# Performance work log

Measured on AMD Instinct MI355X. Metric: run time of the kernel, lower is better.

The kernel has to match this reference:

```python
import jax, jax.numpy as jnp
import numpy as np

N_NODES = 65536
IN_DIM = 256
HIDDEN = 256
NUM_GRAPHS = 128   # B = batch.max()+1; fixed by construction in setup_inputs
MAX_LEN = 1024     # >= max per-graph length (avg 512, binomial tail << 1024)


def _uniform(key, shape, scale):
    return jax.random.uniform(key, shape, jnp.float32, -scale, scale)


def setup_inputs() -> dict:
    key = jax.random.key(0)
    ks = jax.random.split(key, 12)
    x = jax.random.normal(ks[0], (N_NODES, IN_DIM), jnp.float32)
    batch = jnp.sort(jax.random.randint(ks[1], (N_NODES,), 0, NUM_GRAPHS)).astype(jnp.int64)
    s = 1.0 / np.sqrt(HIDDEN)  # torch nn.GRU init: U(-1/sqrt(H), 1/sqrt(H))
    # gate order follows torch: (r, z, n) stacked along first axis -> 3H rows
    params = {
        'W_ih0': _uniform(ks[2], (3 * HIDDEN, IN_DIM), s),
        'W_hh0': _uniform(ks[3], (3 * HIDDEN, HIDDEN), s),
        'b_ih0': _uniform(ks[4], (3 * HIDDEN,), s),
        'b_hh0': _uniform(ks[5], (3 * HIDDEN,), s),
        'W_ih1': _uniform(ks[6], (3 * HIDDEN, HIDDEN), s),
        'W_hh1': _uniform(ks[7], (3 * HIDDEN, HIDDEN), s),
        'b_ih1': _uniform(ks[8], (3 * HIDDEN,), s),
        'b_hh1': _uniform(ks[9], (3 * HIDDEN,), s),
    }
    return {'x': x, 'batch': batch, **params}


def _gru_layer(xs, W_ih, W_hh, b_ih, b_hh):
    # xs: [B, L, D] -> [B, L, H]; torch GRU cell math, gate order (r, z, n)
    B = xs.shape[0]
    H = W_hh.shape[1]
    gx = jnp.einsum('bld,gd->blg', xs, W_ih) + b_ih  # precompute input gates, one big GEMM

    def step(h, gx_t):
        gh = h @ W_hh.T + b_hh
        xr, xz, xn = jnp.split(gx_t, 3, axis=-1)
        hr, hz, hn = jnp.split(gh, 3, axis=-1)
        r = jax.nn.sigmoid(xr + hr)
        z = jax.nn.sigmoid(xz + hz)
        n = jnp.tanh(xn + r * hn)
        h_new = (1.0 - z) * n + z * h
        return h_new, h_new

    h0 = jnp.zeros((B, H), xs.dtype)
    _, hs = jax.lax.scan(step, h0, jnp.swapaxes(gx, 0, 1))  # [L, B, H]
    return jnp.swapaxes(hs, 0, 1)


def reference(x, batch, W_ih0, W_hh0, b_ih0, b_hh0, W_ih1, W_hh1, b_ih1, b_hh1):
    # Ragged per-graph sequences -> padded [B, MAX_LEN, D]. Padding is at the
    # end of each row; GRU is causal so valid positions match the per-graph
    # loop in the original module exactly, and the masked mean ignores padding.
    N, D = x.shape
    b32 = batch.astype(jnp.int32)
    counts = jax.ops.segment_sum(jnp.ones((N,), jnp.float32), b32, num_segments=NUM_GRAPHS)
    starts = jnp.cumsum(counts) - counts              # exclusive prefix sum
    pos = jnp.arange(N, dtype=jnp.float32) - starts[b32]
    pos = pos.astype(jnp.int32)                       # position within graph

    xp = jnp.zeros((NUM_GRAPHS, MAX_LEN, D), x.dtype).at[b32, pos].set(x)
    mask = jnp.zeros((NUM_GRAPHS, MAX_LEN), x.dtype).at[b32, pos].set(1.0)

    h = _gru_layer(xp, W_ih0, W_hh0, b_ih0, b_hh0)
    h = _gru_layer(h, W_ih1, W_hh1, b_ih1, b_hh1)

    denom = jnp.maximum(counts, 1.0)[:, None]
    out = jnp.sum(h * mask[:, :, None], axis=1) / denom  # mean over valid steps
    return out  # dropout is identity at eval
```

## Files before the change

kernel.cpp:

```cpp
#include <hip/hip_runtime.h>
#include <hip/hip_bf16.h>

typedef _Float16 half2_t __attribute__((ext_vector_type(2)));
typedef _Float16 f16x8   __attribute__((ext_vector_type(8)));
typedef float    f32x4   __attribute__((ext_vector_type(4)));
typedef unsigned short u16;
typedef unsigned int   u32;

#define N_NODES 65536
#define IN_DIM  256
#define HIDDEN  256
#define G3      768
#define NGRAPH  128

__device__ __forceinline__ float sigf(float x)    { return 1.f / (1.f + __expf(-x)); }
__device__ __forceinline__ float tanhfast(float x){ return 2.f / (1.f + __expf(-2.f * x)) - 1.f; }

__global__ void k_starts(const int* __restrict__ batch, int* __restrict__ starts, int n, int ngraph) {
    int g = blockIdx.x * blockDim.x + threadIdx.x;
    if (g > ngraph) return;
    int stride = (batch[n - 1] == 0) ? 2 : 1;
    if (g == ngraph) { starts[g] = n; return; }
    int lo = 0, hi = n;
    while (lo < hi) { int mid = (lo + hi) >> 1; if (batch[(size_t)mid * stride] < g) lo = mid + 1; else hi = mid; }
    starts[g] = lo;
}

__global__ void k_cvt8(const float* __restrict__ s, u16* __restrict__ d, int n) {
    int t = blockIdx.x * 256 + threadIdx.x;
    int i = t * 8;
    if (i >= n) return;
    float4 a = ((const float4*)(s + i))[0];
    float4 b = ((const float4*)(s + i))[1];
    f16x8 o;
    o[0] = (_Float16)a.x; o[1] = (_Float16)a.y; o[2] = (_Float16)a.z; o[3] = (_Float16)a.w;
    o[4] = (_Float16)b.x; o[5] = (_Float16)b.y; o[6] = (_Float16)b.z; o[7] = (_Float16)b.w;
    *(f16x8*)(d + i) = o;
}

__global__ void k_swz(const float* __restrict__ W, uint4* __restrict__ out) {
    int t = blockIdx.x * 256 + threadIdx.x;
    if (t >= 24576) return;
    int l = t & 63, i = (t >> 6) & 15, rest = t >> 10;
    int wv = rest / 3, rg = rest % 3;
    int row = rg * 256 + (wv & 3) * 64 + l;
    int col = (wv >> 2) * 128 + i * 8;
    const float* s = W + row * 256 + col;
    f16x8 o;
#pragma unroll
    for (int q = 0; q < 8; q++) o[q] = (_Float16)s[q];
    out[t] = __builtin_bit_cast(uint4, o);
}

template <typename AT>
__global__ __launch_bounds__(256) void k_gemm(
    const AT* __restrict__ A, const u16* __restrict__ Bm,
    const float* __restrict__ bias, u16* __restrict__ C,
    int M, int N, int K)
{
    __shared__ u16 As[128 * 40];
    __shared__ u16 Bs[128 * 40];
    const int m0 = blockIdx.y * 128, n0 = blockIdx.x * 128;
    const int t = threadIdx.x;
    const int wave = t >> 6, lane = t & 63;
    const int wm = wave & 1, wn = wave >> 1;
    const int lr = lane & 15, lq = lane >> 4;
    f32x4 acc[4][4] = {};
    const int sr = t >> 1, sp = t & 1;
    const AT*  gA = A  + (size_t)(m0 + sr) * K + sp * 16;
    const u16* gB = Bm + (size_t)(n0 + sr) * K + sp * 16;
    u16* sA = As + sr * 40 + sp * 16;
    u16* sB = Bs + sr * 40 + sp * 16;
    for (int kt = 0; kt < K; kt += 32) {
        uint4 av0, av1;
        if constexpr (sizeof(AT) == 4) {
            float4 a0 = ((const float4*)gA)[0], a1 = ((const float4*)gA)[1];
            float4 a2 = ((const float4*)gA)[2], a3 = ((const float4*)gA)[3];
            f16x8 lo, hi;
            lo[0]=(_Float16)a0.x; lo[1]=(_Float16)a0.y; lo[2]=(_Float16)a0.z; lo[3]=(_Float16)a0.w;
            lo[4]=(_Float16)a1.x; lo[5]=(_Float16)a1.y; lo[6]=(_Float16)a1.z; lo[7]=(_Float16)a1.w;
            hi[0]=(_Float16)a2.x; hi[1]=(_Float16)a2.y; hi[2]=(_Float16)a2.z; hi[3]=(_Float16)a2.w;
            hi[4]=(_Float16)a3.x; hi[5]=(_Float16)a3.y; hi[6]=(_Float16)a3.z; hi[7]=(_Float16)a3.w;
            av0 = __builtin_bit_cast(uint4, lo);
            av1 = __builtin_bit_cast(uint4, hi);
        } else {
            av0 = ((const uint4*)gA)[0];
            av1 = ((const uint4*)gA)[1];
        }
        uint4 b0 = ((const uint4*)gB)[0], b1 = ((const uint4*)gB)[1];
        gA += 32; gB += 32;
        __syncthreads();
        ((uint4*)sA)[0] = av0; ((uint4*)sA)[1] = av1;
        ((uint4*)sB)[0] = b0;  ((uint4*)sB)[1] = b1;
        __syncthreads();
        f16x8 af[4], bf[4];
#pragma unroll
        for (int i = 0; i < 4; i++)
            af[i] = *(const f16x8*)(As + (wm * 64 + i * 16 + lr) * 40 + lq * 8);
#pragma unroll
        for (int j = 0; j < 4; j++)
            bf[j] = *(const f16x8*)(Bs + (wn * 64 + j * 16 + lr) * 40 + lq * 8);
#pragma unroll
        for (int i = 0; i < 4; i++)
#pragma unroll
            for (int j = 0; j < 4; j++)
                acc[i][j] = __builtin_amdgcn_mfma_f32_16x16x32_f16(af[i], bf[j], acc[i][j], 0, 0, 0);
    }
#pragma unroll
    for (int i = 0; i < 4; i++) {
        int row = m0 + wm * 64 + i * 16 + lq * 4;
#pragma unroll
        for (int j = 0; j < 4; j++) {
            int col = n0 + wn * 64 + j * 16 + lr;
            float bv = bias[col];
#pragma unroll
            for (int rr = 0; rr < 4; rr++) {
                _Float16 v = (_Float16)(acc[i][j][rr] + bv);
                C[(size_t)(row + rr) * N + col] = __builtin_bit_cast(u16, v);
            }
        }
    }
}

__global__ __launch_bounds__(512) __attribute__((amdgpu_waves_per_eu(2, 2)))
void k_rec(
    const u16* __restrict__ gx,
    const uint4* __restrict__ wsw,
    const float* __restrict__ bhh,
    const int*   __restrict__ starts,
    u16* __restrict__ hout,
    float* __restrict__ out)
{
    __shared__ float4 part1[HIDDEN];
    __shared__ uint4 hpk4[HIDDEN / 8];
    const int g = blockIdx.x;
    const int tid = threadIdx.x;
    const int h = tid & 255;
    const int q = tid >> 8;
    const int start = starts[g];
    const int len = starts[g + 1] - start;
    if (tid < HIDDEN / 8) hpk4[tid] = make_uint4(0, 0, 0, 0);
    uint4 w[3][16];
    {
        const int wv = tid >> 6, l = tid & 63;
#pragma unroll
        for (int rg = 0; rg < 3; rg++)
#pragma unroll
            for (int i = 0; i < 16; i++) {
                uint4 v = wsw[(size_t)(((wv * 3 + rg) * 16 + i) * 64 + l)];
                asm volatile("" : "+v"(v.x), "+v"(v.y), "+v"(v.z), "+v"(v.w));
                w[rg][i] = v;
            }
    }
    const _Float16* gxb = (const _Float16*)gx + (size_t)start * G3;
    u16* hb = hout ? (hout + (size_t)start * HIDDEN + h) : (u16*)nullptr;
    float hp = 0.f, hs = 0.f;
    float gr = 0.f, gz = 0.f, gn = 0.f;
    float br = 0.f, bz = 0.f, bn = 0.f;
    if (q == 0) {
        br = bhh[h]; bz = bhh[h + 256]; bn = bhh[h + 512];
        if (len > 0) {
            const _Float16* p = gxb + h;
            gr = (float)p[0]; gz = (float)p[256]; gn = (float)p[512];
        }
    }
    const int qb = q * 16;
    __syncthreads();
    for (int t = 0; t < len; ++t) {
        float pr = 0.f, pz = 0.f, pn = 0.f;
        if (q == 0) {
            int tn = t + 1 < len ? t + 1 : len - 1;
            const _Float16* p = gxb + ((u32)tn * G3 + h);
            pr = (float)p[0]; pz = (float)p[256]; pn = (float)p[512];
        }
        float ar = 0.f, az = 0.f, an = 0.f;
#pragma unroll
        for (int i = 0; i < 16; i++) {
            uint4 hv = hpk4[qb + i];
            half2_t hx = __builtin_bit_cast(half2_t, hv.x), hy = __builtin_bit_cast(half2_t, hv.y);
            half2_t hz2 = __builtin_bit_cast(half2_t, hv.z), hw = __builtin_bit_cast(half2_t, hv.w);
            ar = __builtin_amdgcn_fdot2(__builtin_bit_cast(half2_t, w[0][i].x), hx, ar, false);
            az = __builtin_amdgcn_fdot2(__builtin_bit_cast(half2_t, w[1][i].x), hx, az, false);
            an = __builtin_amdgcn_fdot2(__builtin_bit_cast(half2_t, w[2][i].x), hx, an, false);
            ar = __builtin_amdgcn_fdot2(__builtin_bit_cast(half2_t, w[0][i].y), hy, ar, false);
            az = __builtin_amdgcn_fdot2(__builtin_bit_cast(half2_t, w[1][i].y), hy, az, false);
            an = __builtin_amdgcn_fdot2(__builtin_bit_cast(half2_t, w[2][i].y), hy, an, false);
            ar = __builtin_amdgcn_fdot2(__builtin_bit_cast(half2_t, w[0][i].z), hz2, ar, false);
            az = __builtin_amdgcn_fdot2(__builtin_bit_cast(half2_t, w[1][i].z), hz2, az, false);
            an = __builtin_amdgcn_fdot2(__builtin_bit_cast(half2_t, w[2][i].z), hz2, an, false);
            ar = __builtin_amdgcn_fdot2(__builtin_bit_cast(half2_t, w[0][i].w), hw, ar, false);
            az = __builtin_amdgcn_fdot2(__builtin_bit_cast(half2_t, w[1][i].w), hw, az, false);
            an = __builtin_amdgcn_fdot2(__builtin_bit_cast(half2_t, w[2][i].w), hw, an, false);
        }
        if (q) part1[h] = make_float4(ar, az, an, 0.f);
        __syncthreads();
        if (!q) {
            float4 p = part1[h];
            float sr = ar + p.x + br;
            float sz = az + p.y + bz;
            float sn = an + p.z + bn;
            float r = sigf(gr + sr);
            float z = sigf(gz + sz);
            float n = tanhfast(gn + r * sn);
            float hnew = (1.f - z) * n + z * hp;
            hp = hnew; hs += hnew;
            _Float16 ph = (_Float16)hnew;
            u16 pk = __builtin_bit_cast(u16, ph);
            ((u16*)hpk4)[h] = pk;
            if (hb) hb[(u32)t * HIDDEN] = pk;
            gr = pr; gz = pz; gn = pn;
        }
        __syncthreads();
    }
    if (out && !q) {
        float inv = 1.f / (float)(len > 0 ? len : 1);
        out[g * HIDDEN + h] = hs * inv;
    }
}

extern "C" void kernel_launch(void* const* d_in, const int* in_sizes, int n_in,
                              void* d_out, int out_size, void* d_ws, size_t ws_size,
                              hipStream_t stream)
{
    const float* x     = (const float*)d_in[0];
    const int*   batch = (const int*)d_in[1];
    const float* Wih0  = (const float*)d_in[2];
    const float* Whh0  = (const float*)d_in[3];
    const float* bih0  = (const float*)d_in[4];
    const float* bhh0  = (const float*)d_in[5];
    const float* Wih1  = (const float*)d_in[6];
    const float* Whh1  = (const float*)d_in[7];
    const float* bih1  = (const float*)d_in[8];
    const float* bhh1  = (const float*)d_in[9];
    float* out = (float*)d_out;

    char* ws = (char*)d_ws;
    size_t o = 0;
    int*   starts = (int*)  (ws + o); o += 4096;
    u16*   wi0    = (u16*)  (ws + o); o += (size_t)G3 * IN_DIM * 2;
    u16*   wi1    = (u16*)  (ws + o); o += (size_t)G3 * HIDDEN * 2;
    uint4* wsw0   = (uint4*)(ws + o); o += (size_t)G3 * HIDDEN * 2;
    uint4* wsw1   = (uint4*)(ws + o); o += (size_t)G3 * HIDDEN * 2;
    u16*   h0     = (u16*)  (ws + o); o += (size_t)N_NODES * HIDDEN * 2;
    u16*   gxbuf  = (u16*)  (ws + o); o += (size_t)N_NODES * G3 * 2;

    k_starts<<<1, 256, 0, stream>>>(batch, starts, N_NODES, NGRAPH);
    k_cvt8<<<96, 256, 0, stream>>>(Wih0, wi0, G3 * IN_DIM);
    k_cvt8<<<96, 256, 0, stream>>>(Wih1, wi1, G3 * HIDDEN);
    k_swz<<<96, 256, 0, stream>>>(Whh0, wsw0);
    k_swz<<<96, 256, 0, stream>>>(Whh1, wsw1);

    k_gemm<float><<<dim3(G3 / 128, N_NODES / 128), 256, 0, stream>>>(x, wi0, bih0, gxbuf, N_NODES, G3, IN_DIM);
    k_rec<<<NGRAPH, 512, 0, stream>>>(gxbuf, wsw0, bhh0, starts, h0, (float*)nullptr);
    k_gemm<_Float16><<<dim3(G3 / 128, N_NODES / 128), 256, 0, stream>>>((const _Float16*)h0, wi1, bih1, gxbuf, N_NODES, G3, HIDDEN);
    k_rec<<<NGRAPH, 512, 0, stream>>>(gxbuf, wsw1, bhh1, starts, (u16*)nullptr, out);
}
```

Measured before the change: 1.606 ms.

## Use MFMA for GRU recurrent matvec with AGPR-resident weights and folded biases

The per-step recurrent matvec h·W_hh^T is moved from fdot2 accumulation on split thread halves to MFMA 16x16x32 f16 instructions. All 8 waves compute 96 gate rows each, with weights held in accumulation registers and written to a shared gates buffer. The W_hh swizzle is changed to the MFMA A-operand layout, and the r/z hidden biases are folded into the input-GEMM bias through a small new kernel. Prefetching of next-step gx is dropped, and the MFMA computes a 16-column product of which only one column is used, so much of its work is wasted.

Measured after the change: 1.718 ms. +7.0%, slower.

```diff
diff --git a/kernel.cpp b/kernel.cpp
--- a/kernel.cpp
+++ b/kernel.cpp
@@ -38,13 +38,18 @@
     *(f16x8*)(d + i) = o;
 }
 
+__global__ void k_bias(const float* __restrict__ bih, const float* __restrict__ bhh, float* __restrict__ o) {
+    int i = blockIdx.x * 256 + threadIdx.x;
+    if (i < G3) o[i] = bih[i] + (i < 512 ? bhh[i] : 0.f);
+}
+
 __global__ void k_swz(const float* __restrict__ W, uint4* __restrict__ out) {
     int t = blockIdx.x * 256 + threadIdx.x;
     if (t >= 24576) return;
-    int l = t & 63, i = (t >> 6) & 15, rest = t >> 10;
-    int wv = rest / 3, rg = rest % 3;
-    int row = rg * 256 + (wv & 3) * 64 + l;
-    int col = (wv >> 2) * 128 + i * 8;
+    int l = t & 63, kt = (t >> 6) & 7, rest = t >> 9;
+    int wv = rest / 6, t6 = rest % 6;
+    int row = wv * 96 + t6 * 16 + (l & 15);
+    int col = kt * 32 + (l >> 4) * 8;
     const float* s = W + row * 256 + col;
     f16x8 o;
 #pragma unroll
@@ -131,90 +136,71 @@
     u16* __restrict__ hout,
     float* __restrict__ out)
 {
-    __shared__ float4 part1[HIDDEN];
+    __shared__ float gates[G3];
     __shared__ uint4 hpk4[HIDDEN / 8];
     const int g = blockIdx.x;
     const int tid = threadIdx.x;
-    const int h = tid & 255;
-    const int q = tid >> 8;
+    const int l = tid & 63, wv = tid >> 6;
     const int start = starts[g];
     const int len = starts[g + 1] - start;
     if (tid < HIDDEN / 8) hpk4[tid] = make_uint4(0, 0, 0, 0);
-    uint4 w[3][16];
+    f16x8 wA[6][8];
     {
-        const int wv = tid >> 6, l = tid & 63;
-#pragma unroll
-        for (int rg = 0; rg < 3; rg++)
-#pragma unroll
-            for (int i = 0; i < 16; i++) {
-                uint4 v = wsw[(size_t)(((wv * 3 + rg) * 16 + i) * 64 + l)];
-                asm volatile("" : "+v"(v.x), "+v"(v.y), "+v"(v.z), "+v"(v.w));
-                w[rg][i] = v;
+        const uint4* p = wsw + (size_t)wv * 48 * 64 + l;
+#pragma unroll
+        for (int t6 = 0; t6 < 6; t6++)
+#pragma unroll
+            for (int kt = 0; kt < 8; kt++) {
+                f16x8 v = __builtin_bit_cast(f16x8, p[(t6 * 8 + kt) * 64]);
+                asm volatile("" : "+a"(v));
+                wA[t6][kt] = v;
             }
     }
-    const _Float16* gxb = (const _Float16*)gx + (size_t)start * G3;
-    u16* hb = hout ? (hout + (size_t)start * HIDDEN + h) : (u16*)nullptr;
+    const _Float16* gxr = (const _Float16*)gx + (size_t)start * G3 + (tid & 255);
+    u16* hb = hout ? (hout + (size_t)start * HIDDEN + (tid & 255)) : (u16*)nullptr;
     float hp = 0.f, hs = 0.f;
-    float gr = 0.f, gz = 0.f, gn = 0.f;
-    float br = 0.f, bz = 0.f, bn = 0.f;
-    if (q == 0) {
-        br = bhh[h]; bz = bhh[h + 256]; bn = bhh[h + 512];
-        if (len > 0) {
-            const _Float16* p = gxb + h;
-            gr = (float)p[0]; gz = (float)p[256]; gn = (float)p[512];
-        }
-    }
-    const int qb = q * 16;
+    const float bn = (tid < 256) ? bhh[512 + tid] : 0.f;
     __syncthreads();
     for (int t = 0; t < len; ++t) {
-        float pr = 0.f, pz = 0.f, pn = 0.f;
-        if (q == 0) {
-            int tn = t + 1 < len ? t + 1 : len - 1;
-            const _Float16* p = gxb + ((u32)tn * G3 + h);
-            pr = (float)p[0]; pz = (float)p[256]; pn = (float)p[512];
-        }
-        float ar = 0.f, az = 0.f, an = 0.f;
-#pragma unroll
-        for (int i = 0; i < 16; i++) {
-            uint4 hv = hpk4[qb + i];
-            half2_t hx = __builtin_bit_cast(half2_t, hv.x), hy = __builtin_bit_cast(half2_t, hv.y);
-            half2_t hz2 = __builtin_bit_cast(half2_t, hv.z), hw = __builtin_bit_cast(half2_t, hv.w);
-            ar = __builtin_amdgcn_fdot2(__builtin_bit_cast(half2_t, w[0][i].x), hx, ar, false);
-            az = __builtin_amdgcn_fdot2(__builtin_bit_cast(half2_t, w[1][i].x), hx, az, false);
-            an = __builtin_amdgcn_fdot2(__builtin_bit_cast(half2_t, w[2][i].x), hx, an, false);
-            ar = __builtin_amdgcn_fdot2(__builtin_bit_cast(half2_t, w[0][i].y), hy, ar, false);
-            az = __builtin_amdgcn_fdot2(__builtin_bit_cast(half2_t, w[1][i].y), hy, az, false);
-            an = __builtin_amdgcn_fdot2(__builtin_bit_cast(half2_t, w[2][i].y), hy, an, false);
-            ar = __builtin_amdgcn_fdot2(__builtin_bit_cast(half2_t, w[0][i].z), hz2, ar, false);
-            az = __builtin_amdgcn_fdot2(__builtin_bit_cast(half2_t, w[1][i].z), hz2, az, false);
-            an = __builtin_amdgcn_fdot2(__builtin_bit_cast(half2_t, w[2][i].z), hz2, an, false);
-            ar = __builtin_amdgcn_fdot2(__builtin_bit_cast(half2_t, w[0][i].w), hw, ar, false);
-            az = __builtin_amdgcn_fdot2(__builtin_bit_cast(half2_t, w[1][i].w), hw, az, false);
-            an = __builtin_amdgcn_fdot2(__builtin_bit_cast(half2_t, w[2][i].w), hw, an, false);
-        }
-        if (q) part1[h] = make_float4(ar, az, an, 0.f);
-        __syncthreads();
-        if (!q) {
-            float4 p = part1[h];
-            float sr = ar + p.x + br;
-            float sz = az + p.y + bz;
-            float sn = an + p.z + bn;
-            float r = sigf(gr + sr);
-            float z = sigf(gz + sz);
-            float n = tanhfast(gn + r * sn);
+        float gr = 0.f, gz = 0.f, gn = 0.f;
+        if (tid < 256) {
+            const _Float16* p = gxr + (size_t)t * G3;
+            gr = (float)p[0]; gz = (float)p[256]; gn = (float)p[512];
+        }
+        f32x4 acc[6];
+#pragma unroll
+        for (int t6 = 0; t6 < 6; t6++) acc[t6] = (f32x4){0.f, 0.f, 0.f, 0.f};
+#pragma unroll
+        for (int kt = 0; kt < 8; kt++) {
+            f16x8 b = __builtin_bit_cast(f16x8, hpk4[kt * 4 + (l >> 4)]);
+#pragma unroll
+            for (int t6 = 0; t6 < 6; t6++)
+                acc[t6] = __builtin_amdgcn_mfma_f32_16x16x32_f16(wA[t6][kt], b, acc[t6], 0, 0, 0);
+        }
+        if ((l & 15) == 0) {
+            int ro = wv * 96 + (l >> 4) * 4;
+#pragma unroll
+            for (int t6 = 0; t6 < 6; t6++)
+                *(f32x4*)&gates[ro + t6 * 16] = acc[t6];
+        }
+        __syncthreads();
+        if (tid < 256) {
+            int h = tid;
+            float r = sigf(gr + gates[h]);
+            float z = sigf(gz + gates[256 + h]);
+            float n = tanhfast(gn + r * (gates[512 + h] + bn));
             float hnew = (1.f - z) * n + z * hp;
             hp = hnew; hs += hnew;
             _Float16 ph = (_Float16)hnew;
             u16 pk = __builtin_bit_cast(u16, ph);
             ((u16*)hpk4)[h] = pk;
             if (hb) hb[(u32)t * HIDDEN] = pk;
-            gr = pr; gz = pz; gn = pn;
-        }
-        __syncthreads();
-    }
-    if (out && !q) {
+        }
+        __syncthreads();
+    }
+    if (out && tid < 256) {
         float inv = 1.f / (float)(len > 0 ? len : 1);
-        out[g * HIDDEN + h] = hs * inv;
+        out[g * HIDDEN + tid] = hs * inv;
     }
 }
 
@@ -237,6 +223,8 @@
     char* ws = (char*)d_ws;
     size_t o = 0;
     int*   starts = (int*)  (ws + o); o += 4096;
+    float* bias0  = (float*)(ws + o); o += 4096;
+    float* bias1  = (float*)(ws + o); o += 4096;
     u16*   wi0    = (u16*)  (ws + o); o += (size_t)G3 * IN_DIM * 2;
     u16*   wi1    = (u16*)  (ws + o); o += (size_t)G3 * HIDDEN * 2;
     uint4* wsw0   = (uint4*)(ws + o); o += (size_t)G3 * HIDDEN * 2;
@@ -245,13 +233,15 @@
     u16*   gxbuf  = (u16*)  (ws + o); o += (size_t)N_NODES * G3 * 2;
 
     k_starts<<<1, 256, 0, stream>>>(batch, starts, N_NODES, NGRAPH);
+    k_bias<<<3, 256, 0, stream>>>(bih0, bhh0, bias0);
+    k_bias<<<3, 256, 0, stream>>>(bih1, bhh1, bias1);
     k_cvt8<<<96, 256, 0, stream>>>(Wih0, wi0, G3 * IN_DIM);
     k_cvt8<<<96, 256, 0, stream>>>(Wih1, wi1, G3 * HIDDEN);
     k_swz<<<96, 256, 0, stream>>>(Whh0, wsw0);
     k_swz<<<96, 256, 0, stream>>>(Whh1, wsw1);
 
-    k_gemm<float><<<dim3(G3 / 128, N_NODES / 128), 256, 0, stream>>>(x, wi0, bih0, gxbuf, N_NODES, G3, IN_DIM);
+    k_gemm<float><<<dim3(G3 / 128, N_NODES / 128), 256, 0, stream>>>(x, wi0, bias0, gxbuf, N_NODES, G3, IN_DIM);
     k_rec<<<NGRAPH, 512, 0, stream>>>(gxbuf, wsw0, bhh0, starts, h0, (float*)nullptr);
-    k_gemm<_Float16><<<dim3(G3 / 128, N_NODES / 128), 256, 0, stream>>>((const _Float16*)h0, wi1, bih1, gxbuf, N_NODES, G3, HIDDEN);
+    k_gemm<_Float16><<<dim3(G3 / 128, N_NODES / 128), 256, 0, stream>>>((const _Float16*)h0, wi1, bias1, gxbuf, N_NODES, G3, HIDDEN);
     k_rec<<<NGRAPH, 512, 0, stream>>>(gxbuf, wsw1, bhh1, starts, (u16*)nullptr, out);
 }
```
